# Kernel optimization log

Hardware: AMD Instinct MI355X
Metric: run time of the kernel (lower is better)

The kernel has to match this reference:

```python
import jax, jax.numpy as jnp
import numpy as np

N, D, H, E = 50000, 128, 64, 800000


def _linear_params(key, fan_in, fan_out):
    k1, k2 = jax.random.split(key)
    bound = 1.0 / np.sqrt(fan_in)
    w = jax.random.uniform(k1, (fan_in, fan_out), jnp.float32, -bound, bound)
    b = jax.random.uniform(k2, (fan_out,), jnp.float32, -bound, bound)
    return w, b


def setup_inputs() -> dict:
    key = jax.random.key(0)
    ks = jax.random.split(key, 10)
    node_states = jax.random.normal(ks[0], (N, D), jnp.float32)
    capacities = jax.random.uniform(ks[1], (N,), jnp.float32)
    edge_index = jax.random.randint(ks[2], (2, E), 0, N, jnp.int64)
    # redistribution_net: Linear(2D->H), SiLU, Linear(H->H), SiLU, Linear(H->1)
    rw1, rb1 = _linear_params(ks[3], 2 * D, H)
    rw2, rb2 = _linear_params(ks[4], H, H)
    rw3, rb3 = _linear_params(ks[5], H, 1)
    # protection_net: Linear(D+1->H), SiLU, Linear(H->1)
    pw1, pb1 = _linear_params(ks[6], D + 1, H)
    pw2, pb2 = _linear_params(ks[7], H, 1)
    # post_jump_transform: Linear(D->D), Tanh
    tw, tb = _linear_params(ks[8], D, D)
    return dict(node_states=node_states, capacities=capacities, edge_index=edge_index,
                rw1=rw1, rb1=rb1, rw2=rw2, rb2=rb2, rw3=rw3, rb3=rb3,
                pw1=pw1, pb1=pb1, pw2=pw2, pb2=pb2, tw=tw, tb=tb)


def reference(node_states, capacities, edge_index,
              rw1, rb1, rw2, rb2, rw3, rb3,
              pw1, pb1, pw2, pb2, tw, tb):
    n = node_states.shape[0]
    # --- detect_jumps: protection_net(cat(states, capacities)) > 0 ---
    x = jnp.concatenate([node_states, capacities[:, None]], axis=-1)  # (N, D+1)
    act = (jax.nn.silu(x @ pw1 + pb1) @ pw2 + pb2)[:, 0]              # (N,)
    jump_mask = act > 0.0

    # --- redistribute_load ---
    src, tgt = edge_index[0], edge_index[1]
    src_failed = jump_mask[src]
    tgt_alive = ~jump_mask[tgt]
    emask = src_failed & tgt_alive                                    # (E,)

    wi = jnp.concatenate([node_states[src], node_states[tgt]], axis=-1)  # (E, 2D)
    h = jax.nn.silu(wi @ rw1 + rb1)
    h = jax.nn.silu(h @ rw2 + rb2)
    raw = (h @ rw3 + rb3)[:, 0]                                       # (E,)

    # per-source segment softmax over edges with emask
    raw_m = jnp.where(emask, raw, -jnp.inf)
    seg_max = jax.ops.segment_max(raw_m, src, num_segments=n)
    seg_max = jnp.where(jnp.isfinite(seg_max), seg_max, 0.0)
    e = jnp.where(emask, jnp.exp(raw - seg_max[src]), 0.0)
    denom = jax.ops.segment_sum(e, src, num_segments=n)
    dsrc = denom[src]
    w = e / jnp.where(dsrc > 0, dsrc, 1.0)                            # (E,)

    failed_load = jnp.where(jump_mask[:, None], node_states, 0.0)     # (N, D)
    messages = w[:, None] * failed_load[src]                          # (E, D)
    added = jax.ops.segment_sum(messages, tgt, num_segments=n)        # (N, D)
    redistributed = node_states + added

    # --- apply_jumps: failed nodes -> tanh(Linear(x)) * 0.05 ---
    protected = jnp.tanh(redistributed @ tw + tb) * 0.05
    new_states = jnp.where(jump_mask[:, None], protected, redistributed)
    return new_states, jump_mask
```

## Files before the change

kernel.cpp:

```cpp
#include <hip/hip_runtime.h>
#include <cmath>

#define D 128
#define HID 64

__device__ __forceinline__ float silu_f(float x) { return x / (1.0f + expf(-x)); }

__device__ __forceinline__ float4 fma4(float a, float4 w, float4 c) {
    c.x = fmaf(a, w.x, c.x); c.y = fmaf(a, w.y, c.y);
    c.z = fmaf(a, w.z, c.z); c.w = fmaf(a, w.w, c.w);
    return c;
}
__device__ __forceinline__ float4 silu4(float4 v) {
    v.x = silu_f(v.x); v.y = silu_f(v.y); v.z = silu_f(v.z); v.w = silu_f(v.w);
    return v;
}

#define INIT16(bp) { const float4* _b4 = reinterpret_cast<const float4*>(bp); \
    h0 = _b4[0]; h1 = _b4[1]; h2 = _b4[2]; h3 = _b4[3]; \
    h4 = _b4[4]; h5 = _b4[5]; h6 = _b4[6]; h7 = _b4[7]; \
    h8 = _b4[8]; h9 = _b4[9]; h10 = _b4[10]; h11 = _b4[11]; \
    h12 = _b4[12]; h13 = _b4[13]; h14 = _b4[14]; h15 = _b4[15]; }

#define SILU16() { h0 = silu4(h0); h1 = silu4(h1); h2 = silu4(h2); h3 = silu4(h3); \
    h4 = silu4(h4); h5 = silu4(h5); h6 = silu4(h6); h7 = silu4(h7); \
    h8 = silu4(h8); h9 = silu4(h9); h10 = silu4(h10); h11 = silu4(h11); \
    h12 = silu4(h12); h13 = silu4(h13); h14 = silu4(h14); h15 = silu4(h15); }

__device__ __forceinline__ void fd4(float4 h, float4 w, float& s0, float& s1, float& s2, float& s3) {
    s0 = fmaf(h.x, w.x, s0); s1 = fmaf(h.y, w.y, s1);
    s2 = fmaf(h.z, w.z, s2); s3 = fmaf(h.w, w.w, s3);
}
#define FD16(w4) { fd4(h0, w4[0], s0, s1, s2, s3);  fd4(h1, w4[1], s0, s1, s2, s3);  \
    fd4(h2, w4[2], s0, s1, s2, s3);  fd4(h3, w4[3], s0, s1, s2, s3);  \
    fd4(h4, w4[4], s0, s1, s2, s3);  fd4(h5, w4[5], s0, s1, s2, s3);  \
    fd4(h6, w4[6], s0, s1, s2, s3);  fd4(h7, w4[7], s0, s1, s2, s3);  \
    fd4(h8, w4[8], s0, s1, s2, s3);  fd4(h9, w4[9], s0, s1, s2, s3);  \
    fd4(h10, w4[10], s0, s1, s2, s3); fd4(h11, w4[11], s0, s1, s2, s3); \
    fd4(h12, w4[12], s0, s1, s2, s3); fd4(h13, w4[13], s0, s1, s2, s3); \
    fd4(h14, w4[14], s0, s1, s2, s3); fd4(h15, w4[15], s0, s1, s2, s3); }

__device__ __forceinline__ float accdot(float4 h, float4 w, float act) {
    act = fmaf(silu_f(h.x), w.x, act);
    act = fmaf(silu_f(h.y), w.y, act);
    act = fmaf(silu_f(h.z), w.z, act);
    act = fmaf(silu_f(h.w), w.w, act);
    return act;
}

__global__ void k_prep(const float* __restrict__ rw2, float* __restrict__ rw2T) {
    int i = blockIdx.x * blockDim.x + threadIdx.x;
    if (i < HID * HID) rw2T[i] = rw2[(i & (HID - 1)) * HID + (i >> 6)];
}

__global__ __launch_bounds__(256) void k_node(
    const float* __restrict__ states, const float* __restrict__ caps,
    const float* __restrict__ pw1, const float* __restrict__ pb1,
    const float* __restrict__ pw2, const float* __restrict__ pb2,
    const float* __restrict__ rw1,
    unsigned* __restrict__ mask, unsigned* __restrict__ mlist,
    unsigned* __restrict__ counters, float* __restrict__ outmask,
    float* __restrict__ uv, int N) {
    __shared__ float wl[16384];
    unsigned tid = threadIdx.x;
    {
        const float4* s4 = reinterpret_cast<const float4*>(pw1);
        float4* d4 = reinterpret_cast<float4*>(wl);
#pragma unroll
        for (int q = 0; q < 9; ++q) {
            unsigned idx = tid + q * 256u;
            if (idx < 2064u) d4[idx] = s4[idx];
        }
    }
    __syncthreads();
    unsigned nl = tid >> 2, g = tid & 3u;
    unsigned n = blockIdx.x * 64u + nl;
    bool active = n < (unsigned)N;
    unsigned nq = active ? n : (unsigned)(N - 1);
    const float4* row = reinterpret_cast<const float4*>(states + (size_t)nq * D);
    unsigned m;
    {
        float4 a0, a1, a2, a3;
        { const float4* b4 = reinterpret_cast<const float4*>(pb1 + g * 16);
          a0 = b4[0]; a1 = b4[1]; a2 = b4[2]; a3 = b4[3]; }
        const float* wg = wl + g * 16;
#pragma unroll 4
        for (int kb = 0; kb < 32; ++kb) {
            float4 x = row[kb];
            const float* w = wg + (size_t)kb * 4 * HID;
            const float4* w0 = reinterpret_cast<const float4*>(w);
            const float4* w1 = reinterpret_cast<const float4*>(w + HID);
            const float4* w2q = reinterpret_cast<const float4*>(w + 2 * HID);
            const float4* w3q = reinterpret_cast<const float4*>(w + 3 * HID);
            a0 = fma4(x.x, w0[0], a0); a1 = fma4(x.x, w0[1], a1); a2 = fma4(x.x, w0[2], a2); a3 = fma4(x.x, w0[3], a3);
            a0 = fma4(x.y, w1[0], a0); a1 = fma4(x.y, w1[1], a1); a2 = fma4(x.y, w1[2], a2); a3 = fma4(x.y, w1[3], a3);
            a0 = fma4(x.z, w2q[0], a0); a1 = fma4(x.z, w2q[1], a1); a2 = fma4(x.z, w2q[2], a2); a3 = fma4(x.z, w2q[3], a3);
            a0 = fma4(x.w, w3q[0], a0); a1 = fma4(x.w, w3q[1], a1); a2 = fma4(x.w, w3q[2], a2); a3 = fma4(x.w, w3q[3], a3);
        }
        {
            float xv = caps[nq];
            const float4* wc = reinterpret_cast<const float4*>(wg + (size_t)128 * HID);
            a0 = fma4(xv, wc[0], a0); a1 = fma4(xv, wc[1], a1);
            a2 = fma4(xv, wc[2], a2); a3 = fma4(xv, wc[3], a3);
        }
        const float4* w2 = reinterpret_cast<const float4*>(pw2 + g * 16);
        float p = 0.0f;
        p = accdot(a0, w2[0], p); p = accdot(a1, w2[1], p);
        p = accdot(a2, w2[2], p); p = accdot(a3, w2[3], p);
        p += __shfl_xor(p, 1);
        p += __shfl_xor(p, 2);
        float act = p + pb2[0];
        m = (act > 0.0f) ? 1u : 0u;
        bool pred = false;
        if (active && g == 0) {
            mask[n] = m;
            outmask[n] = m ? 1.0f : 0.0f;
            pred = (m != 0u);
        }
        unsigned lane = tid & 63u;
        unsigned long long bal = __ballot(pred);
        unsigned wcnt = (unsigned)__popcll(bal);
        unsigned pre  = (unsigned)__popcll(bal & ((1ull << lane) - 1ull));
        unsigned base = 0;
        if (lane == 0 && wcnt) base = atomicAdd(&counters[1], wcnt);
        base = __shfl(base, 0);
        if (pred) mlist[base + pre] = n;
    }
    __syncthreads();
    {
        const float4* s4 = reinterpret_cast<const float4*>(rw1);
        float4* d4 = reinterpret_cast<float4*>(wl);
#pragma unroll
        for (int q = 0; q < 16; ++q) d4[tid + q * 256u] = s4[tid + q * 256u];
    }
    __syncthreads();
    if (!active) return;
    const float* wg = wl + (m ? 0u : 8192u) + g * 16;
    float4 a0, a1, a2, a3;
    a0.x=a0.y=a0.z=a0.w=0.f; a1=a0; a2=a0; a3=a0;
#pragma unroll 4
    for (int kb = 0; kb < 32; ++kb) {
        float4 x = row[kb];
        const float* w = wg + (size_t)kb * 4 * HID;
        const float4* w0 = reinterpret_cast<const float4*>(w);
        const float4* w1 = reinterpret_cast<const float4*>(w + HID);
        const float4* w2q = reinterpret_cast<const float4*>(w + 2 * HID);
        const float4* w3q = reinterpret_cast<const float4*>(w + 3 * HID);
        a0 = fma4(x.x, w0[0], a0); a1 = fma4(x.x, w0[1], a1); a2 = fma4(x.x, w0[2], a2); a3 = fma4(x.x, w0[3], a3);
        a0 = fma4(x.y, w1[0], a0); a1 = fma4(x.y, w1[1], a1); a2 = fma4(x.y, w1[2], a2); a3 = fma4(x.y, w1[3], a3);
        a0 = fma4(x.z, w2q[0], a0); a1 = fma4(x.z, w2q[1], a1); a2 = fma4(x.z, w2q[2], a2); a3 = fma4(x.z, w2q[3], a3);
        a0 = fma4(x.w, w3q[0], a0); a1 = fma4(x.w, w3q[1], a1); a2 = fma4(x.w, w3q[2], a2); a3 = fma4(x.w, w3q[3], a3);
    }
    float4* o = reinterpret_cast<float4*>(uv + (size_t)n * HID + g * 16);
    o[0] = a0; o[1] = a1; o[2] = a2; o[3] = a3;
}

__global__ __launch_bounds__(256) void k_compact(
    const int* __restrict__ ei, const unsigned* __restrict__ mask,
    unsigned* __restrict__ act_eid, unsigned* __restrict__ counters,
    unsigned* __restrict__ hist, int E) {
    __shared__ unsigned wbase[4];
    int e = blockIdx.x * 256 + threadIdx.x;
    unsigned wid = threadIdx.x >> 6, lane = threadIdx.x & 63u;
    bool pred = false; int t = 0;
    if (e < E) {
        int s = ei[e]; t = ei[E + e];
        pred = mask[s] && !mask[t];
    }
    unsigned long long bal = __ballot(pred);
    unsigned wcnt = (unsigned)__popcll(bal);
    unsigned pre  = (unsigned)__popcll(bal & ((1ull << lane) - 1ull));
    if (lane == 0) wbase[wid] = wcnt;
    __syncthreads();
    if (threadIdx.x == 0) {
        unsigned c0 = wbase[0], c1 = wbase[1], c2 = wbase[2], c3 = wbase[3];
        unsigned tot = c0 + c1 + c2 + c3;
        unsigned b = tot ? atomicAdd(&counters[0], tot) : 0u;
        wbase[0] = b; wbase[1] = b + c0; wbase[2] = b + c0 + c1; wbase[3] = b + c0 + c1 + c2;
    }
    __syncthreads();
    if (pred) {
        act_eid[wbase[wid] + pre] = (unsigned)e;
        atomicAdd(&hist[t], 1u);
    }
}

__global__ __launch_bounds__(256) void k_scanA(const unsigned* __restrict__ hist,
                                               unsigned* __restrict__ bsum, int N) {
    __shared__ unsigned sm[256];
    unsigned t = threadIdx.x;
    unsigned i = blockIdx.x * 256u + t;
    sm[t] = (i < (unsigned)N) ? hist[i] : 0u;
    __syncthreads();
#pragma unroll
    for (unsigned d = 128; d > 0; d >>= 1) {
        if (t < d) sm[t] += sm[t + d];
        __syncthreads();
    }
    if (t == 0) bsum[blockIdx.x] = sm[0];
}
__global__ __launch_bounds__(256) void k_scanB(const unsigned* __restrict__ bsum,
                                               unsigned* __restrict__ bpre, int nb) {
    __shared__ unsigned sm[256];
    unsigned t = threadIdx.x;
    unsigned v = (t < (unsigned)nb) ? bsum[t] : 0u;
    sm[t] = v;
    __syncthreads();
    for (unsigned d = 1; d < 256; d <<= 1) {
        unsigned x = (t >= d) ? sm[t - d] : 0u;
        __syncthreads();
        sm[t] += x;
        __syncthreads();
    }
    if (t < (unsigned)nb) bpre[t] = sm[t] - v;
}
__global__ __launch_bounds__(256) void k_scanC(const unsigned* __restrict__ hist,
                                               const unsigned* __restrict__ bpre,
                                               unsigned* __restrict__ offs,
                                               unsigned* __restrict__ cursor, int N) {
    __shared__ unsigned sm[256];
    unsigned t = threadIdx.x;
    unsigned i = blockIdx.x * 256u + t;
    unsigned v = (i < (unsigned)N) ? hist[i] : 0u;
    sm[t] = v;
    __syncthreads();
    for (unsigned d = 1; d < 256; d <<= 1) {
        unsigned x = (t >= d) ? sm[t - d] : 0u;
        __syncthreads();
        sm[t] += x;
        __syncthreads();
    }
    unsigned exc = sm[t] - v + bpre[blockIdx.x];
    if (i < (unsigned)N) { offs[i] = exc; cursor[i] = exc; }
    if (i == (unsigned)N - 1) offs[N] = exc + v;
}

__global__ __launch_bounds__(256) void k_edge_mlp(
    const float* __restrict__ uv, const int* __restrict__ ei,
    const float* __restrict__ rb1, const float* __restrict__ rw2T,
    const float* __restrict__ rb2, const float* __restrict__ rw3,
    const float* __restrict__ rb3,
    const unsigned* __restrict__ act_eid, const unsigned* __restrict__ counters,
    float* __restrict__ denom, unsigned* __restrict__ cursor,
    float* __restrict__ wbuf, unsigned* __restrict__ sbuf, int E) {
    unsigned cnt = counters[0];
    if (blockIdx.x * 256u >= cnt) return;
    unsigned tid = threadIdx.x;
    unsigned grp = blockIdx.x * 256u + tid;
    bool active = grp < cnt;
    unsigned gq = active ? grp : (cnt - 1);
    int e = (int)act_eid[gq];
    int s = ei[e], tg = ei[E + e];
    const float4* ur = reinterpret_cast<const float4*>(uv + (size_t)s * HID);
    const float4* vr = reinterpret_cast<const float4*>(uv + (size_t)tg * HID);
    float4 h0, h1, h2, h3, h4, h5, h6, h7, h8, h9, h10, h11, h12, h13, h14, h15;
    INIT16(rb1);
#define ADDUV(hh, i) { float4 _u = ur[i]; float4 _v = vr[i]; \
    hh.x = hh.x + _u.x + _v.x; hh.y = hh.y + _u.y + _v.y; \
    hh.z = hh.z + _u.z + _v.z; hh.w = hh.w + _u.w + _v.w; }
    ADDUV(h0, 0)  ADDUV(h1, 1)  ADDUV(h2, 2)  ADDUV(h3, 3)
    ADDUV(h4, 4)  ADDUV(h5, 5)  ADDUV(h6, 6)  ADDUV(h7, 7)
    ADDUV(h8, 8)  ADDUV(h9, 9)  ADDUV(h10, 10) ADDUV(h11, 11)
    ADDUV(h12, 12) ADDUV(h13, 13) ADDUV(h14, 14) ADDUV(h15, 15)
#undef ADDUV
    SILU16();
    float raw = rb3[0];
#pragma unroll 1
    for (int j = 0; j < HID; ++j) {
        const float4* w4 = reinterpret_cast<const float4*>(rw2T + (size_t)j * HID);
        float s0 = rb2[j], s1 = 0.f, s2 = 0.f, s3 = 0.f;
        FD16(w4);
        float h2v = silu_f((s0 + s1) + (s2 + s3));
        raw = fmaf(h2v, rw3[j], raw);
    }
    if (active) {
        float ev = expf(raw);
        atomicAdd(&denom[s], ev);
        unsigned pos = atomicAdd(&cursor[tg], 1u);
        wbuf[pos] = ev;
        sbuf[pos] = (unsigned)s;
    }
}

__global__ __launch_bounds__(256) void k_gather(
    const float* __restrict__ states, const float* __restrict__ wbuf,
    const unsigned* __restrict__ sbuf, const unsigned* __restrict__ offs,
    const float* __restrict__ denom, const unsigned* __restrict__ mask,
    float* __restrict__ out, int N) {
    unsigned n = blockIdx.x * 4u + (threadIdx.x >> 6);
    unsigned lane = threadIdx.x & 63u;
    if (n >= (unsigned)N) return;
    if (mask[n]) return;
    unsigned start = offs[n], end = offs[n + 1];
    float2 acc = reinterpret_cast<const float2*>(states + (size_t)n * D)[lane];
    for (unsigned i = start; i < end; ++i) {
        unsigned s = sbuf[i];
        float w = wbuf[i] / denom[s];
        float2 sv = reinterpret_cast<const float2*>(states + (size_t)s * D)[lane];
        acc.x = fmaf(w, sv.x, acc.x);
        acc.y = fmaf(w, sv.y, acc.y);
    }
    reinterpret_cast<float2*>(out + (size_t)n * D)[lane] = acc;
}

__global__ __launch_bounds__(256) void k_jump(
    const float* __restrict__ states,
    const float* __restrict__ tw, const float* __restrict__ tb,
    const unsigned* __restrict__ mlist, const unsigned* __restrict__ counters,
    float* __restrict__ out) {
    __shared__ float xs[8][D];
    unsigned cnt = counters[1];
    unsigned base = blockIdx.x * 8u;
    if (base >= cnt || cnt == 0) return;
    unsigned tid = threadIdx.x;
    unsigned d = tid & 127u, r = tid >> 7;
    {
        unsigned j = tid >> 5;
        unsigned c = (tid & 31u) * 4u;
        unsigned slot = base + j; if (slot >= cnt) slot = cnt - 1;
        int nn = (int)mlist[slot];
        *reinterpret_cast<float4*>(&xs[j][c]) =
            *reinterpret_cast<const float4*>(&states[(size_t)nn * D + c]);
    }
    __syncthreads();
    float tbd = tb[d];
    float a0 = tbd, a1 = tbd, a2 = tbd, a3 = tbd;
    const float* x0 = &xs[r * 4 + 0][0];
    const float* x1 = &xs[r * 4 + 1][0];
    const float* x2 = &xs[r * 4 + 2][0];
    const float* x3 = &xs[r * 4 + 3][0];
#pragma unroll 1
    for (int k = 0; k < D; ++k) {
        float w = tw[(size_t)k * D + d];
        a0 = fmaf(x0[k], w, a0);
        a1 = fmaf(x1[k], w, a1);
        a2 = fmaf(x2[k], w, a2);
        a3 = fmaf(x3[k], w, a3);
    }
    float res[4] = {a0, a1, a2, a3};
#pragma unroll
    for (int j2 = 0; j2 < 4; ++j2) {
        unsigned slot = base + r * 4 + j2;
        if (slot < cnt) {
            int nn = (int)mlist[slot];
            out[(size_t)nn * D + d] = tanhf(res[j2]) * 0.05f;
        }
    }
}

extern "C" void kernel_launch(void* const* d_in, const int* in_sizes, int n_in,
                              void* d_out, int out_size, void* d_ws, size_t ws_size,
                              hipStream_t stream) {
    const float* states = (const float*)d_in[0];
    const float* caps   = (const float*)d_in[1];
    const int*   ei     = (const int*)d_in[2];
    const float* rw1 = (const float*)d_in[3];  const float* rb1 = (const float*)d_in[4];
    const float* rw2 = (const float*)d_in[5];  const float* rb2 = (const float*)d_in[6];
    const float* rw3 = (const float*)d_in[7];  const float* rb3 = (const float*)d_in[8];
    const float* pw1 = (const float*)d_in[9];  const float* pb1 = (const float*)d_in[10];
    const float* pw2 = (const float*)d_in[11]; const float* pb2 = (const float*)d_in[12];
    const float* tw  = (const float*)d_in[13]; const float* tb  = (const float*)d_in[14];
    const int N = in_sizes[1];
    const int E = in_sizes[2] / 2;
    float* out = (float*)d_out;
    const int nb = (N + 255) / 256;

    float* uv = out;

    unsigned* ws       = (unsigned*)d_ws;
    unsigned* counters = ws;
    float*    denom    = (float*)(ws + 4);
    unsigned* hist     = ws + 4 + 1 * (size_t)N;
    unsigned* mask     = ws + 4 + 2 * (size_t)N;
    unsigned* mlist    = ws + 4 + 3 * (size_t)N;
    unsigned* offs     = ws + 4 + 4 * (size_t)N;
    unsigned* cursor   = ws + 4 + 5 * (size_t)N + 1;
    unsigned* bsum     = ws + 4 + 6 * (size_t)N + 1;
    unsigned* bpre     = bsum + 256;
    unsigned* act_eid  = bpre + 256;
    float*    wbuf     = (float*)(act_eid + (size_t)E);
    unsigned* sbuf     = act_eid + 2 * (size_t)E;
    float*    rw2T     = (float*)(act_eid + 3 * (size_t)E);

    (void)hipMemsetAsync(d_ws, 0, (size_t)(4 + 2 * (size_t)N) * 4, stream);

    k_prep<<<(HID * HID + 255) / 256, 256, 0, stream>>>(rw2, rw2T);
    k_node<<<(N + 63) / 64, 256, 0, stream>>>(states, caps, pw1, pb1, pw2, pb2, rw1,
                                              mask, mlist, counters, out + (size_t)N * D, uv, N);
    k_compact<<<(E + 255) / 256, 256, 0, stream>>>(ei, mask, act_eid, counters, hist, E);
    k_scanA<<<nb, 256, 0, stream>>>(hist, bsum, N);
    k_scanB<<<1, 256, 0, stream>>>(bsum, bpre, nb);
    k_scanC<<<nb, 256, 0, stream>>>(hist, bpre, offs, cursor, N);
    k_edge_mlp<<<(E + 255) / 256, 256, 0, stream>>>(uv, ei, rb1, rw2T, rb2, rw3, rb3,
                                                    act_eid, counters, denom, cursor,
                                                    wbuf, sbuf, E);
    k_gather<<<(N + 3) / 4, 256, 0, stream>>>(states, wbuf, sbuf, offs, denom, mask, out, N);
    k_jump<<<(N + 7) / 8, 256, 0, stream>>>(states, tw, tb, mlist, counters, out);
}
```

Before: 256.3 us.

## Register-block k_node over four nodes per thread and group nodes by mask

The node kernel now gives each 16-thread group four nodes, with each thread owning four output columns. One shared-memory weight float4 is reused across four node rows instead of each thread streaming sixteen weight float4s for a single node. For the second projection, nodes in a block are permuted so that masked nodes come first, which lets most groups take a uniform-weight fast path, with a slower per-node-base fallback for mixed groups. The cost is a serial permutation step on thread 0, extra barriers, and more global row loads per thread.

```diff
diff --git a/kernel.cpp b/kernel.cpp
--- a/kernel.cpp
+++ b/kernel.cpp
@@ -63,6 +63,8 @@
     float* __restrict__ uv, int N) {
     __shared__ float wl[16384];
     unsigned tid = threadIdx.x;
+    unsigned grp = tid >> 4, r = tid & 15u;
+    unsigned lane = tid & 63u;
     {
         const float4* s4 = reinterpret_cast<const float4*>(pw1);
         float4* d4 = reinterpret_cast<float4*>(wl);
@@ -73,58 +75,95 @@
         }
     }
     __syncthreads();
-    unsigned nl = tid >> 2, g = tid & 3u;
-    unsigned n = blockIdx.x * 64u + nl;
-    bool active = n < (unsigned)N;
-    unsigned nq = active ? n : (unsigned)(N - 1);
-    const float4* row = reinterpret_cast<const float4*>(states + (size_t)nq * D);
-    unsigned m;
+    unsigned nbase = blockIdx.x * 64u + grp * 4u;
+    unsigned N1 = (unsigned)(N - 1);
+    unsigned n0 = min(nbase + 0u, N1), n1 = min(nbase + 1u, N1);
+    unsigned n2 = min(nbase + 2u, N1), n3 = min(nbase + 3u, N1);
+    const float4* r0p = reinterpret_cast<const float4*>(states + (size_t)n0 * D);
+    const float4* r1p = reinterpret_cast<const float4*>(states + (size_t)n1 * D);
+    const float4* r2p = reinterpret_cast<const float4*>(states + (size_t)n2 * D);
+    const float4* r3p = reinterpret_cast<const float4*>(states + (size_t)n3 * D);
+    unsigned m0, m1, m2, m3;
     {
         float4 a0, a1, a2, a3;
-        { const float4* b4 = reinterpret_cast<const float4*>(pb1 + g * 16);
-          a0 = b4[0]; a1 = b4[1]; a2 = b4[2]; a3 = b4[3]; }
-        const float* wg = wl + g * 16;
-#pragma unroll 4
+        { float4 b = *reinterpret_cast<const float4*>(pb1 + r * 4);
+          a0 = b; a1 = b; a2 = b; a3 = b; }
+#pragma unroll 2
         for (int kb = 0; kb < 32; ++kb) {
-            float4 x = row[kb];
-            const float* w = wg + (size_t)kb * 4 * HID;
-            const float4* w0 = reinterpret_cast<const float4*>(w);
-            const float4* w1 = reinterpret_cast<const float4*>(w + HID);
-            const float4* w2q = reinterpret_cast<const float4*>(w + 2 * HID);
-            const float4* w3q = reinterpret_cast<const float4*>(w + 3 * HID);
-            a0 = fma4(x.x, w0[0], a0); a1 = fma4(x.x, w0[1], a1); a2 = fma4(x.x, w0[2], a2); a3 = fma4(x.x, w0[3], a3);
-            a0 = fma4(x.y, w1[0], a0); a1 = fma4(x.y, w1[1], a1); a2 = fma4(x.y, w1[2], a2); a3 = fma4(x.y, w1[3], a3);
-            a0 = fma4(x.z, w2q[0], a0); a1 = fma4(x.z, w2q[1], a1); a2 = fma4(x.z, w2q[2], a2); a3 = fma4(x.z, w2q[3], a3);
-            a0 = fma4(x.w, w3q[0], a0); a1 = fma4(x.w, w3q[1], a1); a2 = fma4(x.w, w3q[2], a2); a3 = fma4(x.w, w3q[3], a3);
+            float4 x0 = r0p[kb], x1 = r1p[kb], x2 = r2p[kb], x3 = r3p[kb];
+            const float* wb = wl + (size_t)kb * 256 + r * 4;
+            float4 w;
+            w = *reinterpret_cast<const float4*>(wb);
+            a0 = fma4(x0.x, w, a0); a1 = fma4(x1.x, w, a1); a2 = fma4(x2.x, w, a2); a3 = fma4(x3.x, w, a3);
+            w = *reinterpret_cast<const float4*>(wb + 64);
+            a0 = fma4(x0.y, w, a0); a1 = fma4(x1.y, w, a1); a2 = fma4(x2.y, w, a2); a3 = fma4(x3.y, w, a3);
+            w = *reinterpret_cast<const float4*>(wb + 128);
+            a0 = fma4(x0.z, w, a0); a1 = fma4(x1.z, w, a1); a2 = fma4(x2.z, w, a2); a3 = fma4(x3.z, w, a3);
+            w = *reinterpret_cast<const float4*>(wb + 192);
+            a0 = fma4(x0.w, w, a0); a1 = fma4(x1.w, w, a1); a2 = fma4(x2.w, w, a2); a3 = fma4(x3.w, w, a3);
         }
         {
-            float xv = caps[nq];
-            const float4* wc = reinterpret_cast<const float4*>(wg + (size_t)128 * HID);
-            a0 = fma4(xv, wc[0], a0); a1 = fma4(xv, wc[1], a1);
-            a2 = fma4(xv, wc[2], a2); a3 = fma4(xv, wc[3], a3);
-        }
-        const float4* w2 = reinterpret_cast<const float4*>(pw2 + g * 16);
-        float p = 0.0f;
-        p = accdot(a0, w2[0], p); p = accdot(a1, w2[1], p);
-        p = accdot(a2, w2[2], p); p = accdot(a3, w2[3], p);
-        p += __shfl_xor(p, 1);
-        p += __shfl_xor(p, 2);
-        float act = p + pb2[0];
-        m = (act > 0.0f) ? 1u : 0u;
-        bool pred = false;
-        if (active && g == 0) {
-            mask[n] = m;
-            outmask[n] = m ? 1.0f : 0.0f;
-            pred = (m != 0u);
-        }
-        unsigned lane = tid & 63u;
-        unsigned long long bal = __ballot(pred);
-        unsigned wcnt = (unsigned)__popcll(bal);
-        unsigned pre  = (unsigned)__popcll(bal & ((1ull << lane) - 1ull));
-        unsigned base = 0;
-        if (lane == 0 && wcnt) base = atomicAdd(&counters[1], wcnt);
-        base = __shfl(base, 0);
-        if (pred) mlist[base + pre] = n;
+            float c0 = caps[n0], c1 = caps[n1], c2 = caps[n2], c3 = caps[n3];
+            float4 wc = *reinterpret_cast<const float4*>(wl + 8192 + r * 4);
+            a0 = fma4(c0, wc, a0); a1 = fma4(c1, wc, a1);
+            a2 = fma4(c2, wc, a2); a3 = fma4(c3, wc, a3);
+        }
+        float4 w2v = *reinterpret_cast<const float4*>(pw2 + r * 4);
+        float p0 = accdot(a0, w2v, 0.f), p1 = accdot(a1, w2v, 0.f);
+        float p2 = accdot(a2, w2v, 0.f), p3 = accdot(a3, w2v, 0.f);
+#pragma unroll
+        for (int mm = 1; mm <= 8; mm <<= 1) {
+            p0 += __shfl_xor(p0, mm); p1 += __shfl_xor(p1, mm);
+            p2 += __shfl_xor(p2, mm); p3 += __shfl_xor(p3, mm);
+        }
+        float pb2v = pb2[0];
+        m0 = (p0 + pb2v > 0.0f) ? 1u : 0u;
+        m1 = (p1 + pb2v > 0.0f) ? 1u : 0u;
+        m2 = (p2 + pb2v > 0.0f) ? 1u : 0u;
+        m3 = (p3 + pb2v > 0.0f) ? 1u : 0u;
+        unsigned* lm = reinterpret_cast<unsigned*>(wl + 8320);
+        bool v0 = nbase + 0u < (unsigned)N, v1 = nbase + 1u < (unsigned)N;
+        bool v2 = nbase + 2u < (unsigned)N, v3 = nbase + 3u < (unsigned)N;
+        if (r == 0) {
+            lm[grp * 4 + 0] = v0 ? m0 : 0u;
+            lm[grp * 4 + 1] = v1 ? m1 : 0u;
+            lm[grp * 4 + 2] = v2 ? m2 : 0u;
+            lm[grp * 4 + 3] = v3 ? m3 : 0u;
+            if (v0) { mask[n0] = m0; outmask[n0] = m0 ? 1.0f : 0.0f; }
+            if (v1) { mask[n1] = m1; outmask[n1] = m1 ? 1.0f : 0.0f; }
+            if (v2) { mask[n2] = m2; outmask[n2] = m2 ? 1.0f : 0.0f; }
+            if (v3) { mask[n3] = m3; outmask[n3] = m3 ? 1.0f : 0.0f; }
+        }
+#define EMIT(vq, mq, nq) { \
+        bool pred = (r == 0) && vq && (mq != 0u); \
+        unsigned long long bal = __ballot(pred); \
+        unsigned wcnt = (unsigned)__popcll(bal); \
+        unsigned pre  = (unsigned)__popcll(bal & ((1ull << lane) - 1ull)); \
+        unsigned base = 0; \
+        if (lane == 0 && wcnt) base = atomicAdd(&counters[1], wcnt); \
+        base = __shfl(base, 0); \
+        if (pred) mlist[base + pre] = nq; }
+        EMIT(v0, m0, n0) EMIT(v1, m1, n1) EMIT(v2, m2, n2) EMIT(v3, m3, n3)
+#undef EMIT
+    }
+    __syncthreads();
+    {
+        unsigned* lm = reinterpret_cast<unsigned*>(wl + 8320);
+        unsigned* perm = reinterpret_cast<unsigned*>(wl + 8384);
+        if (tid == 0) {
+            unsigned k = 0;
+            for (int i = 0; i < 64; ++i) if (lm[i])  perm[k++] = (unsigned)i;
+            for (int i = 0; i < 64; ++i) if (!lm[i]) perm[k++] = (unsigned)i;
+        }
+    }
+    __syncthreads();
+    unsigned l0, l1, l2, l3, q0m, q1m, q2m, q3m;
+    {
+        unsigned* lm = reinterpret_cast<unsigned*>(wl + 8320);
+        unsigned* perm = reinterpret_cast<unsigned*>(wl + 8384);
+        l0 = perm[grp * 4 + 0]; l1 = perm[grp * 4 + 1];
+        l2 = perm[grp * 4 + 2]; l3 = perm[grp * 4 + 3];
+        q0m = lm[l0]; q1m = lm[l1]; q2m = lm[l2]; q3m = lm[l3];
     }
     __syncthreads();
     {
@@ -134,25 +173,59 @@
         for (int q = 0; q < 16; ++q) d4[tid + q * 256u] = s4[tid + q * 256u];
     }
     __syncthreads();
-    if (!active) return;
-    const float* wg = wl + (m ? 0u : 8192u) + g * 16;
+    unsigned pn0 = blockIdx.x * 64u + l0, pn1 = blockIdx.x * 64u + l1;
+    unsigned pn2 = blockIdx.x * 64u + l2, pn3 = blockIdx.x * 64u + l3;
+    bool pv0 = pn0 < (unsigned)N, pv1 = pn1 < (unsigned)N;
+    bool pv2 = pn2 < (unsigned)N, pv3 = pn3 < (unsigned)N;
+    const float4* s0p = reinterpret_cast<const float4*>(states + (size_t)min(pn0, N1) * D);
+    const float4* s1p = reinterpret_cast<const float4*>(states + (size_t)min(pn1, N1) * D);
+    const float4* s2p = reinterpret_cast<const float4*>(states + (size_t)min(pn2, N1) * D);
+    const float4* s3p = reinterpret_cast<const float4*>(states + (size_t)min(pn3, N1) * D);
     float4 a0, a1, a2, a3;
     a0.x=a0.y=a0.z=a0.w=0.f; a1=a0; a2=a0; a3=a0;
-#pragma unroll 4
-    for (int kb = 0; kb < 32; ++kb) {
-        float4 x = row[kb];
-        const float* w = wg + (size_t)kb * 4 * HID;
-        const float4* w0 = reinterpret_cast<const float4*>(w);
-        const float4* w1 = reinterpret_cast<const float4*>(w + HID);
-        const float4* w2q = reinterpret_cast<const float4*>(w + 2 * HID);
-        const float4* w3q = reinterpret_cast<const float4*>(w + 3 * HID);
-        a0 = fma4(x.x, w0[0], a0); a1 = fma4(x.x, w0[1], a1); a2 = fma4(x.x, w0[2], a2); a3 = fma4(x.x, w0[3], a3);
-        a0 = fma4(x.y, w1[0], a0); a1 = fma4(x.y, w1[1], a1); a2 = fma4(x.y, w1[2], a2); a3 = fma4(x.y, w1[3], a3);
-        a0 = fma4(x.z, w2q[0], a0); a1 = fma4(x.z, w2q[1], a1); a2 = fma4(x.z, w2q[2], a2); a3 = fma4(x.z, w2q[3], a3);
-        a0 = fma4(x.w, w3q[0], a0); a1 = fma4(x.w, w3q[1], a1); a2 = fma4(x.w, w3q[2], a2); a3 = fma4(x.w, w3q[3], a3);
-    }
-    float4* o = reinterpret_cast<float4*>(uv + (size_t)n * HID + g * 16);
-    o[0] = a0; o[1] = a1; o[2] = a2; o[3] = a3;
+    if (q0m == q1m && q1m == q2m && q2m == q3m) {
+        const float* base = wl + (q0m ? 0u : 8192u) + r * 4;
+#pragma unroll 2
+        for (int kb = 0; kb < 32; ++kb) {
+            float4 x0 = s0p[kb], x1 = s1p[kb], x2 = s2p[kb], x3 = s3p[kb];
+            const float* wb = base + (size_t)kb * 256;
+            float4 w;
+            w = *reinterpret_cast<const float4*>(wb);
+            a0 = fma4(x0.x, w, a0); a1 = fma4(x1.x, w, a1); a2 = fma4(x2.x, w, a2); a3 = fma4(x3.x, w, a3);
+            w = *reinterpret_cast<const float4*>(wb + 64);
+            a0 = fma4(x0.y, w, a0); a1 = fma4(x1.y, w, a1); a2 = fma4(x2.y, w, a2); a3 = fma4(x3.y, w, a3);
+            w = *reinterpret_cast<const float4*>(wb + 128);
+            a0 = fma4(x0.z, w, a0); a1 = fma4(x1.z, w, a1); a2 = fma4(x2.z, w, a2); a3 = fma4(x3.z, w, a3);
+            w = *reinterpret_cast<const float4*>(wb + 192);
+            a0 = fma4(x0.w, w, a0); a1 = fma4(x1.w, w, a1); a2 = fma4(x2.w, w, a2); a3 = fma4(x3.w, w, a3);
+        }
+    } else {
+        const float* b0 = wl + (q0m ? 0u : 8192u) + r * 4;
+        const float* b1 = wl + (q1m ? 0u : 8192u) + r * 4;
+        const float* b2 = wl + (q2m ? 0u : 8192u) + r * 4;
+        const float* b3 = wl + (q3m ? 0u : 8192u) + r * 4;
+#pragma unroll 1
+        for (int kb = 0; kb < 32; ++kb) {
+            float4 x0 = s0p[kb], x1 = s1p[kb], x2 = s2p[kb], x3 = s3p[kb];
+            size_t o = (size_t)kb * 256;
+#pragma unroll
+            for (int u = 0; u < 4; ++u) {
+                size_t oo = o + (size_t)u * 64;
+                float xv0 = (u == 0) ? x0.x : (u == 1) ? x0.y : (u == 2) ? x0.z : x0.w;
+                float xv1 = (u == 0) ? x1.x : (u == 1) ? x1.y : (u == 2) ? x1.z : x1.w;
+                float xv2 = (u == 0) ? x2.x : (u == 1) ? x2.y : (u == 2) ? x2.z : x2.w;
+                float xv3 = (u == 0) ? x3.x : (u == 1) ? x3.y : (u == 2) ? x3.z : x3.w;
+                a0 = fma4(xv0, *reinterpret_cast<const float4*>(b0 + oo), a0);
+                a1 = fma4(xv1, *reinterpret_cast<const float4*>(b1 + oo), a1);
+                a2 = fma4(xv2, *reinterpret_cast<const float4*>(b2 + oo), a2);
+                a3 = fma4(xv3, *reinterpret_cast<const float4*>(b3 + oo), a3);
+            }
+        }
+    }
+    if (pv0) *reinterpret_cast<float4*>(uv + (size_t)pn0 * HID + r * 4) = a0;
+    if (pv1) *reinterpret_cast<float4*>(uv + (size_t)pn1 * HID + r * 4) = a1;
+    if (pv2) *reinterpret_cast<float4*>(uv + (size_t)pn2 * HID + r * 4) = a2;
+    if (pv3) *reinterpret_cast<float4*>(uv + (size_t)pn3 * HID + r * 4) = a3;
 }
 
 __global__ __launch_bounds__(256) void k_compact(
```

New measurement: 304.4 us. 1.19x slower.
